# Kernel optimization log

Measured on AMD Instinct MI355X. Metric: run time of the kernel, lower is better.

The kernel has to match this reference:

```python
import jax, jax.numpy as jnp
import numpy as np

N_QUBITS = 6
N_QLAYERS = 2
N_ESTEPS = 1
DATA_REUPLOAD = True
IN_DIM = 512
OUT_DIM = 512
BATCH, SEQ = 8, 4096
EPS = 1e-5

H_GATE = (np.array([[1.0, 1.0], [1.0, -1.0]]) / np.sqrt(2.0)).astype(np.complex64)


def _apply_1q(psi, U, wire):
    # psi: [B, 2, 2, ..., 2] (N_QUBITS qubit axes); U: [2,2] or [B,2,2]
    psi = jnp.moveaxis(psi, wire + 1, 1)
    if U.ndim == 3:
        psi = jnp.einsum('bij,bj...->bi...', U, psi)
    else:
        psi = jnp.einsum('ij,bj...->bi...', U, psi)
    return jnp.moveaxis(psi, 1, wire + 1)


def _apply_cnot(psi, ctrl, tgt):
    p0 = jax.lax.index_in_dim(psi, 0, axis=ctrl + 1, keepdims=True)
    p1 = jax.lax.index_in_dim(psi, 1, axis=ctrl + 1, keepdims=True)
    p1 = jnp.flip(p1, axis=tgt + 1)  # X on target where control=1
    return jnp.concatenate([p0, p1], axis=ctrl + 1)


def _ry_mat(t):
    # t: scalar or [B] -> [.,2,2] complex
    c = jnp.cos(0.5 * t)
    s = jnp.sin(0.5 * t)
    m = jnp.stack([jnp.stack([c, -s], -1), jnp.stack([s, c], -1)], -2)
    return m.astype(jnp.complex64)


def _rz_mat(t):
    e = jnp.exp(-0.5j * t.astype(jnp.complex64))
    z = jnp.zeros_like(e)
    return jnp.stack([jnp.stack([e, z], -1), jnp.stack([z, jnp.conj(e)], -1)], -2)


def _rx_mat(t):
    c = jnp.cos(0.5 * t).astype(jnp.complex64)
    s = (-1j) * jnp.sin(0.5 * t).astype(jnp.complex64)
    return jnp.stack([jnp.stack([c, s], -1), jnp.stack([s, c], -1)], -2)


def _quantum(z, weights):
    # z: [B, N_QUBITS] real; weights: [N_QLAYERS, 3, N_QUBITS]
    bsz = z.shape[0]
    ry = jnp.arctan(z)          # [B, n]
    rz = jnp.arctan(z * z)      # [B, n]
    psi = jnp.zeros((bsz, 2 ** N_QUBITS), dtype=jnp.complex64).at[:, 0].set(1.0)
    psi = psi.reshape((bsz,) + (2,) * N_QUBITS)
    # encoding: H, RY(arctan z), RZ(arctan z^2) per qubit
    for i in range(N_QUBITS):
        psi = _apply_1q(psi, jnp.asarray(H_GATE), i)
        psi = _apply_1q(psi, _ry_mat(ry[:, i]), i)
        psi = _apply_1q(psi, _rz_mat(rz[:, i]), i)
    for layer in range(N_QLAYERS):
        # entangling ring(s)
        if N_QUBITS > 1 and N_ESTEPS > 0:
            for k in range(N_ESTEPS):
                for i in range(N_QUBITS):
                    psi = _apply_cnot(psi, i, (i + k + 1) % N_QUBITS)
        # parameterized rotations
        for i in range(N_QUBITS):
            psi = _apply_1q(psi, _rx_mat(weights[layer, 0, i]), i)
            psi = _apply_1q(psi, _ry_mat(weights[layer, 1, i]), i)
            psi = _apply_1q(psi, _rz_mat(weights[layer, 2, i]), i)
        if DATA_REUPLOAD and layer < N_QLAYERS - 1:
            for i in range(N_QUBITS):
                psi = _apply_1q(psi, _ry_mat(ry[:, i]), i)
                psi = _apply_1q(psi, _rz_mat(rz[:, i]), i)
    probs = psi.real ** 2 + psi.imag ** 2  # [B, 2,...,2]
    outs = []
    for i in range(N_QUBITS):
        p = jnp.moveaxis(probs, i + 1, 1).reshape(bsz, 2, -1).sum(-1)
        outs.append(p[:, 0] - p[:, 1])  # <Z_i>
    return jnp.stack(outs, axis=1)  # [B, n]


def setup_inputs() -> dict:
    key = jax.random.key(0)
    ks = jax.random.split(key, 8)
    x = jax.random.normal(ks[0], (BATCH, SEQ, IN_DIM), dtype=jnp.float32)
    entry_w = jax.random.normal(ks[1], (N_QUBITS, IN_DIM), dtype=jnp.float32) / np.sqrt(IN_DIM)
    entry_b = jnp.zeros((N_QUBITS,), jnp.float32)
    exit_w = jax.random.normal(ks[2], (OUT_DIM, N_QUBITS), dtype=jnp.float32) / np.sqrt(N_QUBITS)
    exit_b = jnp.zeros((OUT_DIM,), jnp.float32)
    skip_w = jax.random.normal(ks[3], (OUT_DIM, IN_DIM), dtype=jnp.float32) / np.sqrt(IN_DIM)
    skip_b = jnp.zeros((OUT_DIM,), jnp.float32)
    vqc_w = jax.random.uniform(ks[4], (N_QLAYERS, 3, N_QUBITS), dtype=jnp.float32,
                               minval=0.0, maxval=2.0 * np.pi)
    gamma = jnp.ones((OUT_DIM,), jnp.float32)
    beta = jnp.zeros((OUT_DIM,), jnp.float32)
    return dict(x=x, entry_w=entry_w, entry_b=entry_b, exit_w=exit_w, exit_b=exit_b,
                skip_w=skip_w, skip_b=skip_b, vqc_w=vqc_w, gamma=gamma, beta=beta)


def reference(x, entry_w, entry_b, exit_w, exit_b, skip_w, skip_b, vqc_w, gamma, beta):
    shape = x.shape
    flat = x.reshape(-1, shape[-1])                     # [B*S, in_dim]
    z = flat @ entry_w.T + entry_b                      # [B*S, n_qubits]
    q = _quantum(z, vqc_w)                              # [B*S, n_qubits]
    y = (z + q) @ exit_w.T + exit_b                     # [B*S, out_dim]
    h = y + flat @ skip_w.T + skip_b
    mu = h.mean(-1, keepdims=True)
    var = ((h - mu) ** 2).mean(-1, keepdims=True)
    out = gamma * (h - mu) * jax.lax.rsqrt(var + EPS) + beta
    return out.reshape(*shape[:-1], OUT_DIM)
```

## Files before the change

kernel.cpp:

```cpp
#include <hip/hip_runtime.h>
#include <hip/hip_bf16.h>

typedef unsigned short u16;
typedef unsigned int u32;
typedef __attribute__((ext_vector_type(8))) short bf16x8;
typedef __attribute__((ext_vector_type(4))) float f32x4;
typedef __attribute__((ext_vector_type(16))) float f32x16;

__device__ __forceinline__ u16 f2bf(float f) {
    u32 u = __float_as_uint(f);
    u32 r = (u + 0x7fffu + ((u >> 16) & 1u)) >> 16;
    return (u16)r;
}
__device__ __forceinline__ float sx(float v, int m) { return __shfl_xor(v, m, 64); }

#define MROWS 32768
#define IN_D  512
#define OUT_D 512
#define KP    544
#define NQ    6

#define WS_XBF   0
#define WS_WBF   35651584
#define WS_WTRIG (35651584 + 557056)

__global__ void k_setup(const float* __restrict__ skip_w,
                        const float* __restrict__ exit_w,
                        const float* __restrict__ vqc_w,
                        u16* __restrict__ Wbf,
                        float* __restrict__ wtrig) {
    int n = blockIdx.x;
    int t = threadIdx.x;
    for (int c = t; c < KP; c += 64) {
        float v;
        if (c < 512)      v = skip_w[n * 512 + c];
        else if (c < 518) v = exit_w[n * 6 + (c - 512)];
        else              v = 0.0f;
        Wbf[n * KP + c] = f2bf(v);
    }
    if (blockIdx.x == 0 && t < 12) {
        int l = t / 6, i = t % 6;
        float c0 = cosf(0.5f * vqc_w[l * 18 + i]),      s0 = sinf(0.5f * vqc_w[l * 18 + i]);
        float c1 = cosf(0.5f * vqc_w[l * 18 + 6 + i]),  s1 = sinf(0.5f * vqc_w[l * 18 + 6 + i]);
        float c2 = cosf(0.5f * vqc_w[l * 18 + 12 + i]), s2 = sinf(0.5f * vqc_w[l * 18 + 12 + i]);
        float M00r = c1 * c0, M00i =  s1 * s0;
        float M01r = -s1 * c0, M01i = -c1 * s0;
        float M10r =  s1 * c0, M10i = -c1 * s0;
        float M11r = c1 * c0, M11i = -s1 * s0;
        float* o = wtrig + t * 8;
        o[0] = M00r * c2 + M00i * s2;  o[1] = M00i * c2 - M00r * s2;
        o[2] = M01r * c2 + M01i * s2;  o[3] = M01i * c2 - M01r * s2;
        o[4] = M10r * c2 - M10i * s2;  o[5] = M10i * c2 + M10r * s2;
        o[6] = M11r * c2 - M11i * s2;  o[7] = M11i * c2 + M11r * s2;
    }
}

template<int M>
__device__ __forceinline__ void v_real(f32x16& ar, f32x16& ai,
                                       float g00, float g01, float g10, float g11) {
#pragma unroll
    for (int k = 0; k < 16; ++k) if (!(k & M)) {
        const int k1 = k | M;
        float a0 = ar[k], a1 = ar[k1];
        ar[k]  = g00 * a0 + g01 * a1;
        ar[k1] = g10 * a0 + g11 * a1;
        float b0 = ai[k], b1 = ai[k1];
        ai[k]  = g00 * b0 + g01 * b1;
        ai[k1] = g10 * b0 + g11 * b1;
    }
}
template<int M>
__device__ __forceinline__ void v_rz(f32x16& ar, f32x16& ai, float c, float s) {
#pragma unroll
    for (int k = 0; k < 16; ++k) {
        float u = (k & M) ? -s : s;
        float nr = c * ar[k] + u * ai[k];
        ai[k] = c * ai[k] - u * ar[k];
        ar[k] = nr;
    }
}
template<int M>
__device__ __forceinline__ void v_cplx(f32x16& ar, f32x16& ai,
                                       float2 u00, float2 u01, float2 u10, float2 u11) {
#pragma unroll
    for (int k = 0; k < 16; ++k) if (!(k & M)) {
        const int k1 = k | M;
        float a0r = ar[k], a0i = ai[k], a1r = ar[k1], a1i = ai[k1];
        ar[k]  = u00.x * a0r - u00.y * a0i + u01.x * a1r - u01.y * a1i;
        ai[k]  = u00.x * a0i + u00.y * a0r + u01.x * a1i + u01.y * a1r;
        ar[k1] = u10.x * a0r - u10.y * a0i + u11.x * a1r - u11.y * a1i;
        ai[k1] = u10.x * a0i + u10.y * a0r + u11.x * a1i + u11.y * a1r;
    }
}
template<int CM, int TM>
__device__ __forceinline__ void v_cnot(f32x16& ar, f32x16& ai) {
#pragma unroll
    for (int k = 0; k < 16; ++k) if ((k & CM) && !(k & TM)) {
        const int k1 = k | TM;
        float t = ar[k]; ar[k] = ar[k1]; ar[k1] = t;
        t = ai[k]; ai[k] = ai[k1]; ai[k1] = t;
    }
}
__device__ __forceinline__ void vx_real(f32x16& ar, f32x16& ai, int xm, bool b,
                                        float g00, float g01, float g10, float g11) {
    float gs = b ? g11 : g00, go = b ? g10 : g01;
#pragma unroll
    for (int k = 0; k < 16; ++k) {
        float pr = sx(ar[k], xm), pi = sx(ai[k], xm);
        ar[k] = gs * ar[k] + go * pr;
        ai[k] = gs * ai[k] + go * pi;
    }
}
__device__ __forceinline__ void vx_rz(f32x16& ar, f32x16& ai, bool b, float c, float s) {
    float u = b ? -s : s;
#pragma unroll
    for (int k = 0; k < 16; ++k) {
        float nr = c * ar[k] + u * ai[k];
        ai[k] = c * ai[k] - u * ar[k];
        ar[k] = nr;
    }
}
__device__ __forceinline__ void vx_cplx(f32x16& ar, f32x16& ai, int xm, bool b,
                                        float2 u00, float2 u01, float2 u10, float2 u11) {
    float2 us, uo;
    us.x = b ? u11.x : u00.x; us.y = b ? u11.y : u00.y;
    uo.x = b ? u10.x : u01.x; uo.y = b ? u10.y : u01.y;
#pragma unroll
    for (int k = 0; k < 16; ++k) {
        float pr = sx(ar[k], xm), pi = sx(ai[k], xm);
        float nr = us.x * ar[k] - us.y * ai[k] + uo.x * pr - uo.y * pi;
        ai[k] = us.x * ai[k] + us.y * ar[k] + uo.x * pi + uo.y * pr;
        ar[k] = nr;
    }
}

__global__ __launch_bounds__(256) void k_zq(const float* __restrict__ x,
                                            const float* __restrict__ entry_w,
                                            const float* __restrict__ entry_b,
                                            const float* __restrict__ wtrig,
                                            u16* __restrict__ xbf) {
    const int lane = threadIdx.x & 63;
    const int wid  = threadIdx.x >> 6;
    const int grp  = lane >> 2;
    const int sub  = lane & 3;
    const int row  = blockIdx.x * 64 + wid * 16 + grp;
    const bool b4 = (sub & 1) != 0;
    const bool b5 = (sub & 2) != 0;

    float d[NQ] = {0, 0, 0, 0, 0, 0};
#pragma unroll 4
    for (int i = 0; i < 16; ++i) {
        const float4* xp = (const float4*)(x + (size_t)row * IN_D + i * 32 + sub * 8);
        float4 xa = xp[0], xb = xp[1];
        union { u16 u[8]; uint4 v; } pk;
        pk.u[0] = f2bf(xa.x); pk.u[1] = f2bf(xa.y); pk.u[2] = f2bf(xa.z); pk.u[3] = f2bf(xa.w);
        pk.u[4] = f2bf(xb.x); pk.u[5] = f2bf(xb.y); pk.u[6] = f2bf(xb.z); pk.u[7] = f2bf(xb.w);
        *(uint4*)(xbf + (size_t)row * KP + i * 32 + sub * 8) = pk.v;
#pragma unroll
        for (int j = 0; j < NQ; ++j) {
            const float4* wp = (const float4*)(entry_w + j * IN_D + i * 32 + sub * 8);
            float4 wa = wp[0], wb = wp[1];
            d[j] += xa.x * wa.x + xa.y * wa.y + xa.z * wa.z + xa.w * wa.w
                  + xb.x * wb.x + xb.y * wb.y + xb.z * wb.z + xb.w * wb.w;
        }
    }
    float z[NQ];
#pragma unroll
    for (int j = 0; j < NQ; ++j) {
        d[j] += sx(d[j], 1);
        d[j] += sx(d[j], 2);
        z[j] = d[j] + entry_b[j];
    }

    float cy[NQ], sy[NQ], cz[NQ], szv[NQ];
#pragma unroll
    for (int j = 0; j < NQ; ++j) {
        float zj = z[j];
        float c1 = rsqrtf(1.0f + zj * zj);
        cy[j] = sqrtf(0.5f * (1.0f + c1));
        sy[j] = copysignf(sqrtf(fmaxf(0.5f * (1.0f - c1), 0.0f)), zj);
        float w  = zj * zj;
        float c2 = rsqrtf(1.0f + w * w);
        cz[j] = sqrtf(0.5f * (1.0f + c2));
        szv[j] = sqrtf(fmaxf(0.5f * (1.0f - c2), 0.0f));
    }

    f32x16 ar = 0.0f, ai = 0.0f;
    if (sub == 0) ar[0] = 1.0f;

    const float Kc = 0.70710678118f;
#define ENCR(i) { float g00 = Kc*(cy[i]-sy[i]), g01 = Kc*(cy[i]+sy[i]); \
                  float g10 = Kc*(sy[i]+cy[i]), g11 = Kc*(sy[i]-cy[i]); \
                  v_real<(1 << i)>(ar, ai, g00, g01, g10, g11); \
                  v_rz<(1 << i)>(ar, ai, cz[i], szv[i]); }
    ENCR(0) ENCR(1) ENCR(2) ENCR(3)
#undef ENCR
    { float g00 = Kc*(cy[4]-sy[4]), g01 = Kc*(cy[4]+sy[4]);
      float g10 = Kc*(sy[4]+cy[4]), g11 = Kc*(sy[4]-cy[4]);
      vx_real(ar, ai, 1, b4, g00, g01, g10, g11);
      vx_rz(ar, ai, b4, cz[4], szv[4]); }
    { float g00 = Kc*(cy[5]-sy[5]), g01 = Kc*(cy[5]+sy[5]);
      float g10 = Kc*(sy[5]+cy[5]), g11 = Kc*(sy[5]-cy[5]);
      vx_real(ar, ai, 2, b5, g00, g01, g10, g11);
      vx_rz(ar, ai, b5, cz[5], szv[5]); }

    const float2* wu = (const float2*)wtrig;
#pragma unroll
    for (int l = 0; l < 2; ++l) {
        v_cnot<1, 2>(ar, ai); v_cnot<2, 4>(ar, ai); v_cnot<4, 8>(ar, ai);
#pragma unroll
        for (int k = 0; k < 16; ++k) if (k & 8) {
            ar[k] = sx(ar[k], 1); ai[k] = sx(ai[k], 1);
        }
#pragma unroll
        for (int k = 0; k < 16; ++k) {
            float pr = sx(ar[k], 2); ar[k] = b4 ? pr : ar[k];
            float pi = sx(ai[k], 2); ai[k] = b4 ? pi : ai[k];
        }
#pragma unroll
        for (int k = 0; k < 16; k += 2) {
            float t0r = ar[k], t0i = ai[k];
            ar[k]     = b5 ? ar[k + 1] : ar[k];
            ai[k]     = b5 ? ai[k + 1] : ai[k];
            ar[k + 1] = b5 ? t0r : ar[k + 1];
            ai[k + 1] = b5 ? t0i : ai[k + 1];
        }
#define ROTR(i) { int bx = (l * 6 + i) * 4; \
                  v_cplx<(1 << i)>(ar, ai, wu[bx], wu[bx+1], wu[bx+2], wu[bx+3]); }
        ROTR(0) ROTR(1) ROTR(2) ROTR(3)
#undef ROTR
        { int bx = (l * 6 + 4) * 4; vx_cplx(ar, ai, 1, b4, wu[bx], wu[bx+1], wu[bx+2], wu[bx+3]); }
        { int bx = (l * 6 + 5) * 4; vx_cplx(ar, ai, 2, b5, wu[bx], wu[bx+1], wu[bx+2], wu[bx+3]); }
        if (l == 0) {
#define REUPR(i) { v_real<(1 << i)>(ar, ai, cy[i], -sy[i], sy[i], cy[i]); \
                   v_rz<(1 << i)>(ar, ai, cz[i], szv[i]); }
            REUPR(0) REUPR(1) REUPR(2) REUPR(3)
#undef REUPR
            vx_real(ar, ai, 1, b4, cy[4], -sy[4], sy[4], cy[4]);
            vx_rz(ar, ai, b4, cz[4], szv[4]);
            vx_real(ar, ai, 2, b5, cy[5], -sy[5], sy[5], cy[5]);
            vx_rz(ar, ai, b5, cz[5], szv[5]);
        }
    }

    float e[NQ] = {0, 0, 0, 0, 0, 0};
    float tl = 0.0f;
#pragma unroll
    for (int k = 0; k < 16; ++k) {
        float p = ar[k] * ar[k] + ai[k] * ai[k];
        tl += p;
        e[0] += (k & 1) ? -p : p;
        e[1] += (k & 2) ? -p : p;
        e[2] += (k & 4) ? -p : p;
        e[3] += (k & 8) ? -p : p;
    }
    e[4] = b4 ? -tl : tl;
    e[5] = b5 ? -tl : tl;
#pragma unroll
    for (int j = 0; j < NQ; ++j) {
        e[j] += sx(e[j], 1);
        e[j] += sx(e[j], 2);
    }

    union { u16 u[8]; uint4 v; } t0;
#pragma unroll
    for (int j = 0; j < NQ; ++j) t0.u[j] = f2bf(z[j] + e[j]);
    t0.u[6] = 0; t0.u[7] = 0;
    uint4 tv; tv.x = tv.y = tv.z = tv.w = 0;
    if (sub == 0) tv = t0.v;
    *(uint4*)(xbf + (size_t)row * KP + 512 + sub * 8) = tv;
}

#define SA_STRIDE 552

__global__ __launch_bounds__(512) void k_gemm_ln(const u16* __restrict__ xbf,
                                                 const u16* __restrict__ Wbf,
                                                 const float* __restrict__ skip_b,
                                                 const float* __restrict__ exit_b,
                                                 const float* __restrict__ gamma,
                                                 const float* __restrict__ beta,
                                                 float* __restrict__ out) {
    __shared__ __align__(16) u16 sA[64 * SA_STRIDE];
    __shared__ float ps[8][64][2];
    __shared__ float stats[64][2];

    const int tid  = threadIdx.x;
    const int wid  = tid >> 6;
    const int lane = tid & 63;
    const int q    = lane >> 4;
    const int c16  = lane & 15;
    const int m0   = blockIdx.x * 64;

    {
        int row = tid >> 3, c0 = tid & 7;
        const u16* src = xbf + (size_t)(m0 + row) * KP;
        u16* dst = sA + row * SA_STRIDE;
#pragma unroll
        for (int j = 0; j < 9; ++j) {
            int col = c0 + j * 8;
            if (col < 68) *(uint4*)(dst + col * 8) = *(const uint4*)(src + col * 8);
        }
    }
    __syncthreads();

    f32x4 acc[4][4];
#pragma unroll
    for (int mt = 0; mt < 4; ++mt)
#pragma unroll
        for (int nt = 0; nt < 4; ++nt)
#pragma unroll
            for (int r = 0; r < 4; ++r) acc[mt][nt][r] = 0.0f;

    const u16* bB = Wbf + (size_t)(wid * 64 + c16) * KP + q * 8;
    const u16* aL = sA + c16 * SA_STRIDE + q * 8;

    bf16x8 bcur[4], bnxt[4];
#pragma unroll
    for (int nt = 0; nt < 4; ++nt)
        bcur[nt] = *(const bf16x8*)(bB + (size_t)nt * 16 * KP);

#pragma unroll 1
    for (int ks = 0; ks < 17; ++ks) {
        if (ks < 16) {
#pragma unroll
            for (int nt = 0; nt < 4; ++nt)
                bnxt[nt] = *(const bf16x8*)(bB + (size_t)nt * 16 * KP + (ks + 1) * 32);
        }
        bf16x8 af[4];
#pragma unroll
        for (int mt = 0; mt < 4; ++mt)
            af[mt] = *(const bf16x8*)(aL + mt * 16 * SA_STRIDE + ks * 32);
#pragma unroll
        for (int mt = 0; mt < 4; ++mt)
#pragma unroll
            for (int nt = 0; nt < 4; ++nt)
                acc[mt][nt] = __builtin_amdgcn_mfma_f32_16x16x32_bf16(af[mt], bcur[nt], acc[mt][nt], 0, 0, 0);
#pragma unroll
        for (int nt = 0; nt < 4; ++nt) bcur[nt] = bnxt[nt];
    }

    float bias[4], gg[4], bb[4];
#pragma unroll
    for (int nt = 0; nt < 4; ++nt) {
        int n = wid * 64 + nt * 16 + c16;
        bias[nt] = skip_b[n] + exit_b[n];
        gg[nt] = gamma[n];
        bb[nt] = beta[n];
    }
#pragma unroll
    for (int mt = 0; mt < 4; ++mt)
#pragma unroll
        for (int nt = 0; nt < 4; ++nt)
#pragma unroll
            for (int r = 0; r < 4; ++r) acc[mt][nt][r] += bias[nt];

#pragma unroll
    for (int mt = 0; mt < 4; ++mt)
#pragma unroll
        for (int r = 0; r < 4; ++r) {
            float s1 = 0.0f, s2 = 0.0f;
#pragma unroll
            for (int nt = 0; nt < 4; ++nt) {
                float v = acc[mt][nt][r];
                s1 += v; s2 += v * v;
            }
#pragma unroll
            for (int off = 1; off < 16; off <<= 1) {
                s1 += sx(s1, off);
                s2 += sx(s2, off);
            }
            if (c16 == r) {
                int m = mt * 16 + q * 4 + r;
                ps[wid][m][0] = s1;
                ps[wid][m][1] = s2;
            }
        }
    __syncthreads();
    if (tid < 64) {
        float s1 = 0.0f, s2 = 0.0f;
#pragma unroll
        for (int w2 = 0; w2 < 8; ++w2) { s1 += ps[w2][tid][0]; s2 += ps[w2][tid][1]; }
        float mu  = s1 * (1.0f / 512.0f);
        float var = s2 * (1.0f / 512.0f) - mu * mu;
        stats[tid][0] = mu;
        stats[tid][1] = rsqrtf(var + 1e-5f);
    }
    __syncthreads();

#pragma unroll
    for (int mt = 0; mt < 4; ++mt)
#pragma unroll
        for (int r = 0; r < 4; ++r) {
            int m = mt * 16 + q * 4 + r;
            float mu = stats[m][0], rs = stats[m][1];
#pragma unroll
            for (int nt = 0; nt < 4; ++nt) {
                float v = (acc[mt][nt][r] - mu) * rs * gg[nt] + bb[nt];
                out[(size_t)(m0 + m) * OUT_D + wid * 64 + nt * 16 + c16] = v;
            }
        }
}

extern "C" void kernel_launch(void* const* d_in, const int* in_sizes, int n_in,
                              void* d_out, int out_size, void* d_ws, size_t ws_size,
                              hipStream_t stream) {
    const float* x       = (const float*)d_in[0];
    const float* entry_w = (const float*)d_in[1];
    const float* entry_b = (const float*)d_in[2];
    const float* exit_w  = (const float*)d_in[3];
    const float* exit_b  = (const float*)d_in[4];
    const float* skip_w  = (const float*)d_in[5];
    const float* skip_b  = (const float*)d_in[6];
    const float* vqc_w   = (const float*)d_in[7];
    const float* gamma   = (const float*)d_in[8];
    const float* beta    = (const float*)d_in[9];
    float* out = (float*)d_out;

    char* ws = (char*)d_ws;
    u16*   xbf   = (u16*)(ws + WS_XBF);
    u16*   Wbf   = (u16*)(ws + WS_WBF);
    float* wtrig = (float*)(ws + WS_WTRIG);

    k_setup<<<dim3(512), dim3(64), 0, stream>>>(skip_w, exit_w, vqc_w, Wbf, wtrig);
    k_zq<<<dim3(MROWS / 64), dim3(256), 0, stream>>>(x, entry_w, entry_b, wtrig, xbf);
    k_gemm_ln<<<dim3(MROWS / 64), dim3(512), 0, stream>>>(xbf, Wbf, skip_b, exit_b, gamma, beta, out);
}
```

Measured before the change: 207.8 us.

## Fuse quantum encoder into GEMM+LayerNorm kernel and pre-swizzle weight operand

Merges the z/quantum kernel into the GEMM+LN kernel. Each block now converts its 64 rows of x to bf16 directly into shared memory and runs the 6-qubit simulation there, spread over 8 lanes per row with 8 amplitudes each instead of 4 lanes with 16. This removes the global round trip of the bf16 activation buffer and one kernel launch. The setup kernel also rewrites the weights into an MFMA-fragment-ordered layout so the B loads are contiguous per lane. The cost is that quantum simulation and GEMM no longer overlap across kernels, and the simulation uses more shuffles per row.

Result: faster. 186.6 us (-10.2%).

```diff
diff --git a/kernel.cpp b/kernel.cpp
--- a/kernel.cpp
+++ b/kernel.cpp
@@ -5,7 +5,7 @@
 typedef unsigned int u32;
 typedef __attribute__((ext_vector_type(8))) short bf16x8;
 typedef __attribute__((ext_vector_type(4))) float f32x4;
-typedef __attribute__((ext_vector_type(16))) float f32x16;
+typedef __attribute__((ext_vector_type(8))) float f32x8;
 
 __device__ __forceinline__ u16 f2bf(float f) {
     u32 u = __float_as_uint(f);
@@ -19,26 +19,34 @@
 #define OUT_D 512
 #define KP    544
 #define NQ    6
-
-#define WS_XBF   0
-#define WS_WBF   35651584
-#define WS_WTRIG (35651584 + 557056)
+#define SA_STRIDE 552
+
+#define WS_WOP   0
+#define WS_WTRIG 557056
 
 __global__ void k_setup(const float* __restrict__ skip_w,
                         const float* __restrict__ exit_w,
                         const float* __restrict__ vqc_w,
-                        u16* __restrict__ Wbf,
+                        u16* __restrict__ Wop,
                         float* __restrict__ wtrig) {
-    int n = blockIdx.x;
-    int t = threadIdx.x;
-    for (int c = t; c < KP; c += 64) {
-        float v;
-        if (c < 512)      v = skip_w[n * 512 + c];
-        else if (c < 518) v = exit_w[n * 6 + (c - 512)];
-        else              v = 0.0f;
-        Wbf[n * KP + c] = f2bf(v);
-    }
-    if (blockIdx.x == 0 && t < 12) {
+    const int nblk = blockIdx.x;
+    const int t = threadIdx.x;
+    const int n = nblk * 16 + (t & 15);
+    const int q = t >> 4;
+    for (int ks = 0; ks < 17; ++ks) {
+        union { u16 u[8]; uint4 v; } pk;
+#pragma unroll
+        for (int j = 0; j < 8; ++j) {
+            int k = ks * 32 + q * 8 + j;
+            float v;
+            if (k < 512)      v = skip_w[n * 512 + k];
+            else if (k < 518) v = exit_w[n * 6 + (k - 512)];
+            else              v = 0.0f;
+            pk.u[j] = f2bf(v);
+        }
+        *(uint4*)(Wop + ((size_t)(nblk * 17 + ks) * 64 + t) * 8) = pk.v;
+    }
+    if (nblk == 0 && t < 12) {
         int l = t / 6, i = t % 6;
         float c0 = cosf(0.5f * vqc_w[l * 18 + i]),      s0 = sinf(0.5f * vqc_w[l * 18 + i]);
         float c1 = cosf(0.5f * vqc_w[l * 18 + 6 + i]),  s1 = sinf(0.5f * vqc_w[l * 18 + 6 + i]);
@@ -56,10 +64,10 @@
 }
 
 template<int M>
-__device__ __forceinline__ void v_real(f32x16& ar, f32x16& ai,
-                                       float g00, float g01, float g10, float g11) {
-#pragma unroll
-    for (int k = 0; k < 16; ++k) if (!(k & M)) {
+__device__ __forceinline__ void v8_real(f32x8& ar, f32x8& ai,
+                                        float g00, float g01, float g10, float g11) {
+#pragma unroll
+    for (int k = 0; k < 8; ++k) if (!(k & M)) {
         const int k1 = k | M;
         float a0 = ar[k], a1 = ar[k1];
         ar[k]  = g00 * a0 + g01 * a1;
@@ -70,9 +78,9 @@
     }
 }
 template<int M>
-__device__ __forceinline__ void v_rz(f32x16& ar, f32x16& ai, float c, float s) {
-#pragma unroll
-    for (int k = 0; k < 16; ++k) {
+__device__ __forceinline__ void v8_rz(f32x8& ar, f32x8& ai, float c, float s) {
+#pragma unroll
+    for (int k = 0; k < 8; ++k) {
         float u = (k & M) ? -s : s;
         float nr = c * ar[k] + u * ai[k];
         ai[k] = c * ai[k] - u * ar[k];
@@ -80,10 +88,10 @@
     }
 }
 template<int M>
-__device__ __forceinline__ void v_cplx(f32x16& ar, f32x16& ai,
-                                       float2 u00, float2 u01, float2 u10, float2 u11) {
-#pragma unroll
-    for (int k = 0; k < 16; ++k) if (!(k & M)) {
+__device__ __forceinline__ void v8_cplx(f32x8& ar, f32x8& ai,
+                                        float2 u00, float2 u01, float2 u10, float2 u11) {
+#pragma unroll
+    for (int k = 0; k < 8; ++k) if (!(k & M)) {
         const int k1 = k | M;
         float a0r = ar[k], a0i = ai[k], a1r = ar[k1], a1i = ai[k1];
         ar[k]  = u00.x * a0r - u00.y * a0i + u01.x * a1r - u01.y * a1i;
@@ -93,40 +101,40 @@
     }
 }
 template<int CM, int TM>
-__device__ __forceinline__ void v_cnot(f32x16& ar, f32x16& ai) {
-#pragma unroll
-    for (int k = 0; k < 16; ++k) if ((k & CM) && !(k & TM)) {
+__device__ __forceinline__ void v8_cnot(f32x8& ar, f32x8& ai) {
+#pragma unroll
+    for (int k = 0; k < 8; ++k) if ((k & CM) && !(k & TM)) {
         const int k1 = k | TM;
         float t = ar[k]; ar[k] = ar[k1]; ar[k1] = t;
         t = ai[k]; ai[k] = ai[k1]; ai[k1] = t;
     }
 }
-__device__ __forceinline__ void vx_real(f32x16& ar, f32x16& ai, int xm, bool b,
-                                        float g00, float g01, float g10, float g11) {
+__device__ __forceinline__ void vx8_real(f32x8& ar, f32x8& ai, int xm, bool b,
+                                         float g00, float g01, float g10, float g11) {
     float gs = b ? g11 : g00, go = b ? g10 : g01;
 #pragma unroll
-    for (int k = 0; k < 16; ++k) {
+    for (int k = 0; k < 8; ++k) {
         float pr = sx(ar[k], xm), pi = sx(ai[k], xm);
         ar[k] = gs * ar[k] + go * pr;
         ai[k] = gs * ai[k] + go * pi;
     }
 }
-__device__ __forceinline__ void vx_rz(f32x16& ar, f32x16& ai, bool b, float c, float s) {
+__device__ __forceinline__ void vx8_rz(f32x8& ar, f32x8& ai, bool b, float c, float s) {
     float u = b ? -s : s;
 #pragma unroll
-    for (int k = 0; k < 16; ++k) {
+    for (int k = 0; k < 8; ++k) {
         float nr = c * ar[k] + u * ai[k];
         ai[k] = c * ai[k] - u * ar[k];
         ar[k] = nr;
     }
 }
-__device__ __forceinline__ void vx_cplx(f32x16& ar, f32x16& ai, int xm, bool b,
-                                        float2 u00, float2 u01, float2 u10, float2 u11) {
+__device__ __forceinline__ void vx8_cplx(f32x8& ar, f32x8& ai, int xm, bool b,
+                                         float2 u00, float2 u01, float2 u10, float2 u11) {
     float2 us, uo;
     us.x = b ? u11.x : u00.x; us.y = b ? u11.y : u00.y;
     uo.x = b ? u10.x : u01.x; uo.y = b ? u10.y : u01.y;
 #pragma unroll
-    for (int k = 0; k < 16; ++k) {
+    for (int k = 0; k < 8; ++k) {
         float pr = sx(ar[k], xm), pi = sx(ai[k], xm);
         float nr = us.x * ar[k] - us.y * ai[k] + uo.x * pr - uo.y * pi;
         ai[k] = us.x * ai[k] + us.y * ar[k] + uo.x * pi + uo.y * pr;
@@ -134,31 +142,45 @@
     }
 }
 
-__global__ __launch_bounds__(256) void k_zq(const float* __restrict__ x,
-                                            const float* __restrict__ entry_w,
-                                            const float* __restrict__ entry_b,
-                                            const float* __restrict__ wtrig,
-                                            u16* __restrict__ xbf) {
-    const int lane = threadIdx.x & 63;
-    const int wid  = threadIdx.x >> 6;
-    const int grp  = lane >> 2;
-    const int sub  = lane & 3;
-    const int row  = blockIdx.x * 64 + wid * 16 + grp;
-    const bool b4 = (sub & 1) != 0;
-    const bool b5 = (sub & 2) != 0;
+__global__ __launch_bounds__(512) void k_fused(const float* __restrict__ x,
+                                               const float* __restrict__ entry_w,
+                                               const float* __restrict__ entry_b,
+                                               const float* __restrict__ wtrig,
+                                               const u16* __restrict__ Wop,
+                                               const float* __restrict__ skip_b,
+                                               const float* __restrict__ exit_b,
+                                               const float* __restrict__ gamma,
+                                               const float* __restrict__ beta,
+                                               float* __restrict__ out) {
+    __shared__ __align__(16) u16 sA[64 * SA_STRIDE];
+    __shared__ float ps[8][64][2];
+    __shared__ float stats[64][2];
+
+    const int tid  = threadIdx.x;
+    const int wid  = tid >> 6;
+    const int lane = tid & 63;
+    const int m0   = blockIdx.x * 64;
+
+    const int grp = lane >> 3;
+    const int sub = lane & 7;
+    const int lrow = wid * 8 + grp;
+    const int row = m0 + lrow;
+    const bool b3 = (sub & 1) != 0;
+    const bool b4 = (sub & 2) != 0;
+    const bool b5 = (sub & 4) != 0;
 
     float d[NQ] = {0, 0, 0, 0, 0, 0};
-#pragma unroll 4
-    for (int i = 0; i < 16; ++i) {
-        const float4* xp = (const float4*)(x + (size_t)row * IN_D + i * 32 + sub * 8);
+#pragma unroll
+    for (int i = 0; i < 8; ++i) {
+        const float4* xp = (const float4*)(x + (size_t)row * IN_D + i * 64 + sub * 8);
         float4 xa = xp[0], xb = xp[1];
         union { u16 u[8]; uint4 v; } pk;
         pk.u[0] = f2bf(xa.x); pk.u[1] = f2bf(xa.y); pk.u[2] = f2bf(xa.z); pk.u[3] = f2bf(xa.w);
         pk.u[4] = f2bf(xb.x); pk.u[5] = f2bf(xb.y); pk.u[6] = f2bf(xb.z); pk.u[7] = f2bf(xb.w);
-        *(uint4*)(xbf + (size_t)row * KP + i * 32 + sub * 8) = pk.v;
+        *(uint4*)(sA + lrow * SA_STRIDE + i * 64 + sub * 8) = pk.v;
 #pragma unroll
         for (int j = 0; j < NQ; ++j) {
-            const float4* wp = (const float4*)(entry_w + j * IN_D + i * 32 + sub * 8);
+            const float4* wp = (const float4*)(entry_w + j * IN_D + i * 64 + sub * 8);
             float4 wa = wp[0], wb = wp[1];
             d[j] += xa.x * wa.x + xa.y * wa.y + xa.z * wa.z + xa.w * wa.w
                   + xb.x * wb.x + xb.y * wb.y + xb.z * wb.z + xb.w * wb.w;
@@ -169,6 +191,7 @@
     for (int j = 0; j < NQ; ++j) {
         d[j] += sx(d[j], 1);
         d[j] += sx(d[j], 2);
+        d[j] += sx(d[j], 4);
         z[j] = d[j] + entry_b[j];
     }
 
@@ -185,40 +208,43 @@
         szv[j] = sqrtf(fmaxf(0.5f * (1.0f - c2), 0.0f));
     }
 
-    f32x16 ar = 0.0f, ai = 0.0f;
+    f32x8 ar = 0.0f, ai = 0.0f;
     if (sub == 0) ar[0] = 1.0f;
 
     const float Kc = 0.70710678118f;
 #define ENCR(i) { float g00 = Kc*(cy[i]-sy[i]), g01 = Kc*(cy[i]+sy[i]); \
                   float g10 = Kc*(sy[i]+cy[i]), g11 = Kc*(sy[i]-cy[i]); \
-                  v_real<(1 << i)>(ar, ai, g00, g01, g10, g11); \
-                  v_rz<(1 << i)>(ar, ai, cz[i], szv[i]); }
-    ENCR(0) ENCR(1) ENCR(2) ENCR(3)
+                  v8_real<(1 << i)>(ar, ai, g00, g01, g10, g11); \
+                  v8_rz<(1 << i)>(ar, ai, cz[i], szv[i]); }
+    ENCR(0) ENCR(1) ENCR(2)
 #undef ENCR
-    { float g00 = Kc*(cy[4]-sy[4]), g01 = Kc*(cy[4]+sy[4]);
-      float g10 = Kc*(sy[4]+cy[4]), g11 = Kc*(sy[4]-cy[4]);
-      vx_real(ar, ai, 1, b4, g00, g01, g10, g11);
-      vx_rz(ar, ai, b4, cz[4], szv[4]); }
-    { float g00 = Kc*(cy[5]-sy[5]), g01 = Kc*(cy[5]+sy[5]);
-      float g10 = Kc*(sy[5]+cy[5]), g11 = Kc*(sy[5]-cy[5]);
-      vx_real(ar, ai, 2, b5, g00, g01, g10, g11);
-      vx_rz(ar, ai, b5, cz[5], szv[5]); }
+#define ENCX(i, xm, bb_) { float g00 = Kc*(cy[i]-sy[i]), g01 = Kc*(cy[i]+sy[i]); \
+                           float g10 = Kc*(sy[i]+cy[i]), g11 = Kc*(sy[i]-cy[i]); \
+                           vx8_real(ar, ai, xm, bb_, g00, g01, g10, g11); \
+                           vx8_rz(ar, ai, bb_, cz[i], szv[i]); }
+    ENCX(3, 1, b3) ENCX(4, 2, b4) ENCX(5, 4, b5)
+#undef ENCX
 
     const float2* wu = (const float2*)wtrig;
 #pragma unroll
     for (int l = 0; l < 2; ++l) {
-        v_cnot<1, 2>(ar, ai); v_cnot<2, 4>(ar, ai); v_cnot<4, 8>(ar, ai);
-#pragma unroll
-        for (int k = 0; k < 16; ++k) if (k & 8) {
+        v8_cnot<1, 2>(ar, ai); v8_cnot<2, 4>(ar, ai);
+#pragma unroll
+        for (int k = 0; k < 8; ++k) if (k & 4) {
             ar[k] = sx(ar[k], 1); ai[k] = sx(ai[k], 1);
         }
 #pragma unroll
-        for (int k = 0; k < 16; ++k) {
-            float pr = sx(ar[k], 2); ar[k] = b4 ? pr : ar[k];
-            float pi = sx(ai[k], 2); ai[k] = b4 ? pi : ai[k];
-        }
-#pragma unroll
-        for (int k = 0; k < 16; k += 2) {
+        for (int k = 0; k < 8; ++k) {
+            float pr = sx(ar[k], 2); ar[k] = b3 ? pr : ar[k];
+            float pi = sx(ai[k], 2); ai[k] = b3 ? pi : ai[k];
+        }
+#pragma unroll
+        for (int k = 0; k < 8; ++k) {
+            float pr = sx(ar[k], 4); ar[k] = b4 ? pr : ar[k];
+            float pi = sx(ai[k], 4); ai[k] = b4 ? pi : ai[k];
+        }
+#pragma unroll
+        for (int k = 0; k < 8; k += 2) {
             float t0r = ar[k], t0i = ai[k];
             ar[k]     = b5 ? ar[k + 1] : ar[k];
             ai[k]     = b5 ? ai[k + 1] : ai[k];
@@ -226,83 +252,63 @@
             ai[k + 1] = b5 ? t0i : ai[k + 1];
         }
 #define ROTR(i) { int bx = (l * 6 + i) * 4; \
-                  v_cplx<(1 << i)>(ar, ai, wu[bx], wu[bx+1], wu[bx+2], wu[bx+3]); }
-        ROTR(0) ROTR(1) ROTR(2) ROTR(3)
+                  v8_cplx<(1 << i)>(ar, ai, wu[bx], wu[bx+1], wu[bx+2], wu[bx+3]); }
+        ROTR(0) ROTR(1) ROTR(2)
 #undef ROTR
-        { int bx = (l * 6 + 4) * 4; vx_cplx(ar, ai, 1, b4, wu[bx], wu[bx+1], wu[bx+2], wu[bx+3]); }
-        { int bx = (l * 6 + 5) * 4; vx_cplx(ar, ai, 2, b5, wu[bx], wu[bx+1], wu[bx+2], wu[bx+3]); }
+        { int bx = (l * 6 + 3) * 4; vx8_cplx(ar, ai, 1, b3, wu[bx], wu[bx+1], wu[bx+2], wu[bx+3]); }
+        { int bx = (l * 6 + 4) * 4; vx8_cplx(ar, ai, 2, b4, wu[bx], wu[bx+1], wu[bx+2], wu[bx+3]); }
+        { int bx = (l * 6 + 5) * 4; vx8_cplx(ar, ai, 4, b5, wu[bx], wu[bx+1], wu[bx+2], wu[bx+3]); }
         if (l == 0) {
-#define REUPR(i) { v_real<(1 << i)>(ar, ai, cy[i], -sy[i], sy[i], cy[i]); \
-                   v_rz<(1 << i)>(ar, ai, cz[i], szv[i]); }
-            REUPR(0) REUPR(1) REUPR(2) REUPR(3)
+#define REUPR(i) { v8_real<(1 << i)>(ar, ai, cy[i], -sy[i], sy[i], cy[i]); \
+                   v8_rz<(1 << i)>(ar, ai, cz[i], szv[i]); }
+            REUPR(0) REUPR(1) REUPR(2)
 #undef REUPR
-            vx_real(ar, ai, 1, b4, cy[4], -sy[4], sy[4], cy[4]);
-            vx_rz(ar, ai, b4, cz[4], szv[4]);
-            vx_real(ar, ai, 2, b5, cy[5], -sy[5], sy[5], cy[5]);
-            vx_rz(ar, ai, b5, cz[5], szv[5]);
-        }
-    }
-
-    float e[NQ] = {0, 0, 0, 0, 0, 0};
-    float tl = 0.0f;
-#pragma unroll
-    for (int k = 0; k < 16; ++k) {
+            vx8_real(ar, ai, 1, b3, cy[3], -sy[3], sy[3], cy[3]);
+            vx8_rz(ar, ai, b3, cz[3], szv[3]);
+            vx8_real(ar, ai, 2, b4, cy[4], -sy[4], sy[4], cy[4]);
+            vx8_rz(ar, ai, b4, cz[4], szv[4]);
+            vx8_real(ar, ai, 4, b5, cy[5], -sy[5], sy[5], cy[5]);
+            vx8_rz(ar, ai, b5, cz[5], szv[5]);
+        }
+    }
+
+    float e[NQ];
+    float tl = 0.0f, e0 = 0.0f, e1 = 0.0f, e2 = 0.0f;
+#pragma unroll
+    for (int k = 0; k < 8; ++k) {
         float p = ar[k] * ar[k] + ai[k] * ai[k];
         tl += p;
-        e[0] += (k & 1) ? -p : p;
-        e[1] += (k & 2) ? -p : p;
-        e[2] += (k & 4) ? -p : p;
-        e[3] += (k & 8) ? -p : p;
-    }
+        e0 += (k & 1) ? -p : p;
+        e1 += (k & 2) ? -p : p;
+        e2 += (k & 4) ? -p : p;
+    }
+    e[0] = e0; e[1] = e1; e[2] = e2;
+    e[3] = b3 ? -tl : tl;
     e[4] = b4 ? -tl : tl;
     e[5] = b5 ? -tl : tl;
 #pragma unroll
     for (int j = 0; j < NQ; ++j) {
         e[j] += sx(e[j], 1);
         e[j] += sx(e[j], 2);
-    }
-
-    union { u16 u[8]; uint4 v; } t0;
-#pragma unroll
-    for (int j = 0; j < NQ; ++j) t0.u[j] = f2bf(z[j] + e[j]);
-    t0.u[6] = 0; t0.u[7] = 0;
-    uint4 tv; tv.x = tv.y = tv.z = tv.w = 0;
-    if (sub == 0) tv = t0.v;
-    *(uint4*)(xbf + (size_t)row * KP + 512 + sub * 8) = tv;
-}
-
-#define SA_STRIDE 552
-
-__global__ __launch_bounds__(512) void k_gemm_ln(const u16* __restrict__ xbf,
-                                                 const u16* __restrict__ Wbf,
-                                                 const float* __restrict__ skip_b,
-                                                 const float* __restrict__ exit_b,
-                                                 const float* __restrict__ gamma,
-                                                 const float* __restrict__ beta,
-                                                 float* __restrict__ out) {
-    __shared__ __align__(16) u16 sA[64 * SA_STRIDE];
-    __shared__ float ps[8][64][2];
-    __shared__ float stats[64][2];
-
-    const int tid  = threadIdx.x;
-    const int wid  = tid >> 6;
-    const int lane = tid & 63;
-    const int q    = lane >> 4;
-    const int c16  = lane & 15;
-    const int m0   = blockIdx.x * 64;
-
-    {
-        int row = tid >> 3, c0 = tid & 7;
-        const u16* src = xbf + (size_t)(m0 + row) * KP;
-        u16* dst = sA + row * SA_STRIDE;
-#pragma unroll
-        for (int j = 0; j < 9; ++j) {
-            int col = c0 + j * 8;
-            if (col < 68) *(uint4*)(dst + col * 8) = *(const uint4*)(src + col * 8);
-        }
+        e[j] += sx(e[j], 4);
+    }
+
+    if (sub < 4) {
+        uint4 tv; tv.x = tv.y = tv.z = tv.w = 0;
+        if (sub == 0) {
+            union { u16 u[8]; uint4 v; } t0;
+#pragma unroll
+            for (int j = 0; j < NQ; ++j) t0.u[j] = f2bf(z[j] + e[j]);
+            t0.u[6] = 0; t0.u[7] = 0;
+            tv = t0.v;
+        }
+        *(uint4*)(sA + lrow * SA_STRIDE + 512 + sub * 8) = tv;
     }
     __syncthreads();
 
+    const int q   = lane >> 4;
+    const int c16 = lane & 15;
+
     f32x4 acc[4][4];
 #pragma unroll
     for (int mt = 0; mt < 4; ++mt)
@@ -311,25 +317,22 @@
 #pragma unroll
             for (int r = 0; r < 4; ++r) acc[mt][nt][r] = 0.0f;
 
-    const u16* bB = Wbf + (size_t)(wid * 64 + c16) * KP + q * 8;
-    const u16* aL = sA + c16 * SA_STRIDE + q * 8;
-
     bf16x8 bcur[4], bnxt[4];
 #pragma unroll
     for (int nt = 0; nt < 4; ++nt)
-        bcur[nt] = *(const bf16x8*)(bB + (size_t)nt * 16 * KP);
+        bcur[nt] = *(const bf16x8*)(Wop + ((size_t)((wid * 4 + nt) * 17 + 0) * 64 + lane) * 8);
 
 #pragma unroll 1
     for (int ks = 0; ks < 17; ++ks) {
         if (ks < 16) {
 #pragma unroll
             for (int nt = 0; nt < 4; ++nt)
-                bnxt[nt] = *(const bf16x8*)(bB + (size_t)nt * 16 * KP + (ks + 1) * 32);
+                bnxt[nt] = *(const bf16x8*)(Wop + ((size_t)((wid * 4 + nt) * 17 + ks + 1) * 64 + lane) * 8);
         }
         bf16x8 af[4];
 #pragma unroll
         for (int mt = 0; mt < 4; ++mt)
-            af[mt] = *(const bf16x8*)(aL + mt * 16 * SA_STRIDE + ks * 32);
+            af[mt] = *(const bf16x8*)(sA + (mt * 16 + c16) * SA_STRIDE + ks * 32 + q * 8);
 #pragma unroll
         for (int mt = 0; mt < 4; ++mt)
 #pragma unroll
@@ -417,11 +420,10 @@
     float* out = (float*)d_out;
 
     char* ws = (char*)d_ws;
-    u16*   xbf   = (u16*)(ws + WS_XBF);
-    u16*   Wbf   = (u16*)(ws + WS_WBF);
+    u16*   Wop   = (u16*)(ws + WS_WOP);
     float* wtrig = (float*)(ws + WS_WTRIG);
 
-    k_setup<<<dim3(512), dim3(64), 0, stream>>>(skip_w, exit_w, vqc_w, Wbf, wtrig);
-    k_zq<<<dim3(MROWS / 64), dim3(256), 0, stream>>>(x, entry_w, entry_b, wtrig, xbf);
-    k_gemm_ln<<<dim3(MROWS / 64), dim3(512), 0, stream>>>(xbf, Wbf, skip_b, exit_b, gamma, beta, out);
-}
+    k_setup<<<dim3(32), dim3(64), 0, stream>>>(skip_w, exit_w, vqc_w, Wop, wtrig);
+    k_fused<<<dim3(MROWS / 64), dim3(512), 0, stream>>>(x, entry_w, entry_b, wtrig, Wop,
+                                                        skip_b, exit_b, gamma, beta, out);
+}
```
